# Optimization experiments

Measured on AMD Instinct MI355X. Metric: run time of the kernel, lower is better.

Reference implementation:

```python
import jax, jax.numpy as jnp
import numpy as np

PROX_THRESH = 50.0
NEG_SLOPE = 0.2  # PyG GATConv default leaky_relu slope


def _layer_norm(x, g, b, eps=1e-5):
    m = x.mean(-1, keepdims=True)
    v = x.var(-1, keepdims=True)
    return (x - m) / jnp.sqrt(v + eps) * g + b


def _forward(ego_agent_past, neighbor_agents_past, node_w, node_b, node_ln_g,
             node_ln_b, ego_w, ego_b, ego_ln_g, ego_ln_b, gat_w, gat_asrc,
             gat_adst, gat_b, proj_w, proj_b):
    B = ego_agent_past.shape[0]
    ego_last = ego_agent_past[:, -1, :5]            # [B,5]
    nbr_last = neighbor_agents_past[:, :, -1, :5]   # [B,Nn,5]
    x = jnp.concatenate([ego_last[:, None], nbr_last], axis=1)  # [B,N,5]
    N = x.shape[1]
    dim = node_w.shape[1]
    heads, C = gat_asrc.shape[1], gat_asrc.shape[2]

    # build_graph: edge (j->i) iff dist(i,j) < 50 and i != j; GATConv then
    # adds self-loops, so the diagonal is always connected.
    pos = x[..., :2]
    d2 = jnp.sum((pos[:, :, None, :] - pos[:, None, :, :]) ** 2, axis=-1)  # [B,N,N]
    eye = jnp.eye(N, dtype=bool)
    adj = ((jnp.sqrt(d2) < PROX_THRESH) & ~eye) | eye   # adj[b,i,j]: msg j -> i

    # node features zero-padded from 5 -> 11 columns (as in forward)
    nf = jnp.pad(x, ((0, 0), (0, 0), (0, 11 - x.shape[-1])))
    h_node = _layer_norm(jax.nn.relu(nf @ node_w + node_b), node_ln_g, node_ln_b)
    h_ego = _layer_norm(jax.nn.relu(nf[..., :7] @ ego_w + ego_b), ego_ln_g, ego_ln_b)
    is_ego = (jnp.arange(N) == 0)  # node 0 of every scene is the ego
    h = jnp.where(is_ego[None, :, None], h_ego, h_node)  # [B,N,dim]

    # GATConv layers (eval mode, dropout inactive), concat=True
    for l in range(gat_w.shape[0]):
        wh = (h @ gat_w[l]).reshape(B, N, heads, C)                    # [B,N,H,C]
        a_s = jnp.einsum('bnhc,hc->bnh', wh, gat_asrc[l])              # source term
        a_d = jnp.einsum('bnhc,hc->bnh', wh, gat_adst[l])              # dest term
        # e[b,i,j,h] for edge j->i
        e = jax.nn.leaky_relu(a_s[:, None, :, :] + a_d[:, :, None, :], NEG_SLOPE)
        e = jnp.where(adj[..., None], e, -1e9)
        alpha = jax.nn.softmax(e, axis=2)                              # over sources j
        out = jnp.einsum('bijh,bjhc->bihc', alpha, wh).reshape(B, N, dim) + gat_b[l]
        h = jax.nn.relu(out)

    h = h @ proj_w + proj_b
    # all agents are valid (randn features have nonzero abs-sum), so no padding
    mask = jnp.zeros((B, N), dtype=bool)
    return h, mask


def setup_inputs() -> dict:
    key = jax.random.key(0)
    ks = jax.random.split(key, 10)
    B, Nn, T = 16, 1023, 20
    dim, heads, L = 256, 4, 2
    C = dim // heads
    f = lambda i, s: jax.random.normal(ks[i], s, dtype=jnp.float32)
    return {
        'ego_agent_past': f(0, (B, T, 7)),
        'neighbor_agents_past': f(1, (B, Nn, T, 11)),
        'node_w': f(2, (11, dim)) * 0.1, 'node_b': jnp.zeros((dim,), jnp.float32),
        'node_ln_g': jnp.ones((dim,), jnp.float32), 'node_ln_b': jnp.zeros((dim,), jnp.float32),
        'ego_w': f(3, (7, dim)) * 0.1, 'ego_b': jnp.zeros((dim,), jnp.float32),
        'ego_ln_g': jnp.ones((dim,), jnp.float32), 'ego_ln_b': jnp.zeros((dim,), jnp.float32),
        'gat_w': f(4, (L, dim, dim)) * 0.1,
        'gat_asrc': f(5, (L, heads, C)) * 0.1,
        'gat_adst': f(6, (L, heads, C)) * 0.1,
        'gat_b': jnp.zeros((L, dim), jnp.float32),
        'proj_w': f(7, (dim, dim)) * 0.1, 'proj_b': jnp.zeros((dim,), jnp.float32),
    }


def reference(ego_agent_past, neighbor_agents_past, node_w, node_b, node_ln_g,
              node_ln_b, ego_w, ego_b, ego_ln_g, ego_ln_b, gat_w, gat_asrc,
              gat_adst, gat_b, proj_w, proj_b):
    return _forward(ego_agent_past, neighbor_agents_past, node_w, node_b,
                    node_ln_g, node_ln_b, ego_w, ego_b, ego_ln_g, ego_ln_b,
                    gat_w, gat_asrc, gat_adst, gat_b, proj_w, proj_b)
```

## Files before the change

kernel.cpp:

```cpp
#include <hip/hip_runtime.h>
#include <cstddef>

typedef _Float16 f16;
typedef _Float16 f16x8 __attribute__((ext_vector_type(8)));
typedef _Float16 f16x4 __attribute__((ext_vector_type(4)));
typedef __fp16 fp16x2 __attribute__((ext_vector_type(2)));
typedef float f32x4 __attribute__((ext_vector_type(4)));

#define BATCH 16
#define NAGENT 1024
#define NNBR 1023
#define TSTEP 20
#define DIM 256
#define ROWS 16384
#define TH2 2500.0f
#define LOG2E 1.44269504089f

#define O_PX   0
#define O_PY   16384
#define O_H16  32768
#define O_AS   2129920
#define O_AD   2195456
#define O_M    2260992
#define O_US   2261056
#define O_UD   2263104
#define O_WT   2265152
#define O_ADJ  2363456

__global__ __launch_bounds__(256) void node_embed(
    const float* __restrict__ ego, const float* __restrict__ nbr,
    const float* __restrict__ node_w, const float* __restrict__ node_b,
    const float* __restrict__ node_g, const float* __restrict__ node_beta,
    const float* __restrict__ ego_w, const float* __restrict__ ego_b,
    const float* __restrict__ ego_g, const float* __restrict__ ego_beta,
    f16* __restrict__ h16, float* __restrict__ px, float* __restrict__ py) {
    int w = threadIdx.x >> 6, lane = threadIdx.x & 63;
    int row = blockIdx.x * 4 + w;
    int b = row >> 10, n = row & 1023;
    const float* src;
    if (n == 0) src = ego + (size_t)b * TSTEP * 7 + (TSTEP - 1) * 7;
    else        src = nbr + (((size_t)b * NNBR + (n - 1)) * TSTEP + (TSTEP - 1)) * 11;
    const float *W, *bias, *g, *beta;
    if (n == 0) { W = ego_w;  bias = ego_b;  g = ego_g;  beta = ego_beta; }
    else        { W = node_w; bias = node_b; g = node_g; beta = node_beta; }
    float xv[5];
#pragma unroll
    for (int k = 0; k < 5; k++) xv[k] = src[k];
    if (lane == 0) { px[row] = xv[0]; py[row] = xv[1]; }
    int c0 = lane * 4;
    float4 bv = *(const float4*)(bias + c0);
    float acc[4] = {bv.x, bv.y, bv.z, bv.w};
#pragma unroll
    for (int k = 0; k < 5; k++) {
        float4 wv = *(const float4*)(W + (size_t)k * 256 + c0);
        acc[0] = fmaf(xv[k], wv.x, acc[0]);
        acc[1] = fmaf(xv[k], wv.y, acc[1]);
        acc[2] = fmaf(xv[k], wv.z, acc[2]);
        acc[3] = fmaf(xv[k], wv.w, acc[3]);
    }
#pragma unroll
    for (int c = 0; c < 4; c++) acc[c] = fmaxf(acc[c], 0.f);
    float s1 = acc[0] + acc[1] + acc[2] + acc[3];
    float s2 = acc[0]*acc[0] + acc[1]*acc[1] + acc[2]*acc[2] + acc[3]*acc[3];
#pragma unroll
    for (int off = 1; off < 64; off <<= 1) {
        s1 += __shfl_xor(s1, off);
        s2 += __shfl_xor(s2, off);
    }
    float mean = s1 * (1.f / 256.f);
    float var  = s2 * (1.f / 256.f) - mean * mean;
    float rstd = rsqrtf(var + 1e-5f);
    float4 gv = *(const float4*)(g + c0);
    float4 be = *(const float4*)(beta + c0);
    f16x4 o;
    o[0] = (f16)((acc[0] - mean) * rstd * gv.x + be.x);
    o[1] = (f16)((acc[1] - mean) * rstd * gv.y + be.y);
    o[2] = (f16)((acc[2] - mean) * rstd * gv.z + be.z);
    o[3] = (f16)((acc[3] - mean) * rstd * gv.w + be.w);
    *(f16x4*)(h16 + (size_t)row * 256 + c0) = o;
}

__global__ __launch_bounds__(256) void adj_build(const float* __restrict__ px,
                                                 const float* __restrict__ py,
                                                 unsigned char* __restrict__ mask) {
    int blk = blockIdx.x;
    int b = blk >> 6, ic = blk & 63;
    int base = b << 10;
    __shared__ float sx[1024], sy[1024];
    int t = threadIdx.x;
#pragma unroll
    for (int i = 0; i < 4; i++) {
        sx[t + i * 256] = px[base + t + i * 256];
        sy[t + i * 256] = py[base + t + i * 256];
    }
    __syncthreads();
    int i_loc = t >> 4;
    int s = (t >> 3) & 1;
    int q = (t >> 1) & 3;
    int chalf = t & 1;
    int ig = ic * 16 + i_loc;
    float xi = sx[ig], yi = sy[ig];
    unsigned int w0 = 0, w1 = 0;
#pragma unroll
    for (int cc = 0; cc < 8; cc++) {
        int c = chalf * 8 + cc;
        unsigned int byte = 0;
        int j0 = s * 512 + c * 32 + q * 8;
#pragma unroll
        for (int jj = 0; jj < 8; jj++) {
            int j = j0 + jj;
            float dx = sx[j] - xi, dy = sy[j] - yi;
            if ((dx * dx + dy * dy < TH2) || (j == ig)) byte |= 1u << jj;
        }
        if (cc < 4) w0 |= byte << (cc * 8);
        else        w1 |= byte << ((cc - 4) * 8);
    }
    uint2 v; v.x = w0; v.y = w1;
    *(uint2*)(mask + (((size_t)(base + ig)) << 7) + s * 64 + q * 16 + chalf * 8) = v;
}

__global__ __launch_bounds__(256) void prep_weights(
    const float* __restrict__ gat_w, const float* __restrict__ proj_w,
    const float* __restrict__ asrc, const float* __restrict__ adst,
    f16* __restrict__ WT, float* __restrict__ us, float* __restrict__ ud) {
    int bid = blockIdx.x;
    int t = threadIdx.x;
    if (bid < 48) {
        int m = bid >> 4, part = bid & 15;
        const float* W = (m < 2) ? (gat_w + (size_t)m * 65536) : proj_w;
        f16* WO = WT + (size_t)m * 65536;
#pragma unroll
        for (int i = 0; i < 2; i++) {
            int chunk = part * 512 + i * 256 + t;
            int lane = chunk & 63;
            int ksnt = chunk >> 6;
            int ks = ksnt & 7, nt = ksnt >> 3;
            int n = nt * 16 + (lane & 15);
            int k0 = ks * 32 + (lane >> 4) * 8;
            f16x8 v;
#pragma unroll
            for (int e = 0; e < 8; e++) v[e] = (f16)W[(size_t)(k0 + e) * 256 + n];
            *(f16x8*)(WO + (size_t)chunk * 8) = v;
        }
    } else {
        int blk = bid - 48;
        int l = blk >> 2, h = blk & 3;
        const float* W  = gat_w + (size_t)l * 65536 + t * 256 + h * 64;
        const float* as = asrc + l * 256 + h * 64;
        const float* ad = adst + l * 256 + h * 64;
        float s = 0.f, d = 0.f;
#pragma unroll 8
        for (int c = 0; c < 64; c++) { s = fmaf(W[c], as[c], s); d = fmaf(W[c], ad[c], d); }
        us[blk * 256 + t] = s;
        ud[blk * 256 + t] = d;
    }
}

__global__ __launch_bounds__(256, 4) void gemm_f16(
    const f16* __restrict__ A, const f16* __restrict__ BT2,
    f16* __restrict__ whT, float* __restrict__ outF, const float* __restrict__ bias,
    const float* __restrict__ us, const float* __restrict__ ud,
    float* __restrict__ a_sT, float* __restrict__ a_dT) {
    __shared__ f16 sA[32 * 264];
    __shared__ float sU[8 * 256];
    int t = threadIdx.x;
    int m0 = blockIdx.x * 32;
    {
        int r = t >> 3, u0 = (t & 7) * 4;
        const f16* gp = A + (size_t)(m0 + r) * 256 + u0 * 8;
        f16* lp = sA + r * 264 + u0 * 8;
#pragma unroll
        for (int u = 0; u < 4; u++)
            *(f16x8*)(lp + u * 8) = *(const f16x8*)(gp + u * 8);
    }
    if (us) {
#pragma unroll
        for (int i = 0; i < 4; i++) sU[t + i * 256] = us[t + i * 256];
#pragma unroll
        for (int i = 0; i < 4; i++) sU[1024 + t + i * 256] = ud[t + i * 256];
    }
    __syncthreads();
    int w = t >> 6, lane = t & 63, il = lane & 15, q = lane >> 4;
    int n0 = w * 64;
    f32x4 acc[2][4];
#pragma unroll
    for (int mt = 0; mt < 2; mt++)
#pragma unroll
        for (int nt = 0; nt < 4; nt++) acc[mt][nt] = (f32x4){0.f, 0.f, 0.f, 0.f};
    const f16* Bp  = BT2 + (size_t)w * 16384 + (size_t)lane * 8;
    const f16* Ap0 = sA + il * 264 + q * 8;
#pragma unroll 2
    for (int ksi = 0; ksi < 8; ksi++) {
        f16x8 a0 = *(const f16x8*)(Ap0 + ksi * 32);
        f16x8 a1 = *(const f16x8*)(Ap0 + 16 * 264 + ksi * 32);
        f16x8 b0 = *(const f16x8*)(Bp + ksi * 512);
        f16x8 b1 = *(const f16x8*)(Bp + 4096 + ksi * 512);
        f16x8 b2 = *(const f16x8*)(Bp + 8192 + ksi * 512);
        f16x8 b3 = *(const f16x8*)(Bp + 12288 + ksi * 512);
        acc[0][0] = __builtin_amdgcn_mfma_f32_16x16x32_f16(a0, b0, acc[0][0], 0, 0, 0);
        acc[0][1] = __builtin_amdgcn_mfma_f32_16x16x32_f16(a0, b1, acc[0][1], 0, 0, 0);
        acc[0][2] = __builtin_amdgcn_mfma_f32_16x16x32_f16(a0, b2, acc[0][2], 0, 0, 0);
        acc[0][3] = __builtin_amdgcn_mfma_f32_16x16x32_f16(a0, b3, acc[0][3], 0, 0, 0);
        acc[1][0] = __builtin_amdgcn_mfma_f32_16x16x32_f16(a1, b0, acc[1][0], 0, 0, 0);
        acc[1][1] = __builtin_amdgcn_mfma_f32_16x16x32_f16(a1, b1, acc[1][1], 0, 0, 0);
        acc[1][2] = __builtin_amdgcn_mfma_f32_16x16x32_f16(a1, b2, acc[1][2], 0, 0, 0);
        acc[1][3] = __builtin_amdgcn_mfma_f32_16x16x32_f16(a1, b3, acc[1][3], 0, 0, 0);
    }
    if (whT) {
        size_t tbase = ((size_t)blockIdx.x) * 512 + (size_t)(w * 4) * 512 * 512 + (size_t)(lane & 15) * 0;
#pragma unroll
        for (int mt = 0; mt < 2; mt++)
#pragma unroll
            for (int nt = 0; nt < 4; nt++) {
                f16x4 v;
#pragma unroll
                for (int reg = 0; reg < 4; reg++) v[reg] = (f16)acc[mt][nt][reg];
                size_t off = ((size_t)(w * 4 + nt) * 512 + blockIdx.x) * 512
                           + (size_t)((mt * 2 + (q >> 1)) * 16 + il) * 8 + (q & 1) * 4;
                *(f16x4*)(whT + off) = v;
            }
        (void)tbase;
    } else {
#pragma unroll
        for (int nt = 0; nt < 4; nt++) {
            float bv = bias[n0 + nt * 16 + il];
#pragma unroll
            for (int mt = 0; mt < 2; mt++)
#pragma unroll
                for (int reg = 0; reg < 4; reg++)
                    outF[(size_t)(m0 + mt * 16 + q * 4 + reg) * 256 + n0 + nt * 16 + il] =
                        acc[mt][nt][reg] + bv;
        }
    }
    if (us) {
        int r2 = t >> 3, sub = t & 7;
        int hh = sub & 3, isD = sub >> 2;
        const float* uv = sU + isD * 1024 + hh * 256;
        const f16* ar = sA + r2 * 264;
        float d0 = 0.f;
#pragma unroll 4
        for (int kk = 0; kk < 32; kk++) {
            f16x8 av = *(const f16x8*)(ar + kk * 8);
            float4 u0 = *(const float4*)(uv + kk * 8);
            float4 u1 = *(const float4*)(uv + kk * 8 + 4);
            d0 += (float)av[0] * u0.x + (float)av[1] * u0.y +
                  (float)av[2] * u0.z + (float)av[3] * u0.w +
                  (float)av[4] * u1.x + (float)av[5] * u1.y +
                  (float)av[6] * u1.z + (float)av[7] * u1.w;
        }
        float* dst = isD ? a_dT : a_sT;
        dst[(size_t)hh * ROWS + m0 + r2] = d0;
    }
}

__global__ __launch_bounds__(256) void reduce_max(const float* __restrict__ a_sT,
                                                  float* __restrict__ M) {
    int blk = blockIdx.x;
    int b = blk >> 2, h = blk & 3;
    const float* p = a_sT + (size_t)h * ROWS + b * NAGENT;
    int t = threadIdx.x;
    float m = fmaxf(fmaxf(p[t], p[t + 256]), fmaxf(p[t + 512], p[t + 768]));
#pragma unroll
    for (int off = 32; off > 0; off >>= 1) m = fmaxf(m, __shfl_down(m, off));
    __shared__ float red[4];
    if ((t & 63) == 0) red[t >> 6] = m;
    __syncthreads();
    if (t == 0) M[blk] = fmaxf(fmaxf(red[0], red[1]), fmaxf(red[2], red[3]));
}

__global__ __launch_bounds__(512, 4) void gat_attn(
    const f16* __restrict__ whT, const float* __restrict__ a_sT,
    const float* __restrict__ a_dT, const unsigned char* __restrict__ mask,
    const float* __restrict__ M, const float* __restrict__ gat_b,
    f16* __restrict__ h16out) {
    __shared__ f32x4 comb[10][4][64];
    int t = threadIdx.x;
    int w = t >> 6, lane = t & 63;
    int h = w & 3, s = w >> 2;
    int B = blockIdx.x;
    int slot = B >> 3;
    int b = (B & 7) + 8 * (slot >> 5);
    int i0 = (slot & 31) << 5;
    int base = b << 10;
    int il = lane & 15, q = lane >> 4;
    int ig0 = i0 + il, ig1 = i0 + 16 + il;

    float Mh = M[b * 4 + h];
    float adv0 = a_dT[(size_t)h * ROWS + base + ig0];
    float adv1 = a_dT[(size_t)h * ROWS + base + ig1];
    float mz0 = Mh + adv0, mz1 = Mh + adv1;
    float mi0 = fmaxf(mz0, 0.2f * mz0), mi1 = fmaxf(mz1, 0.2f * mz1);
    float nm0 = -mi0 * LOG2E, nm1 = -mi1 * LOG2E;

    uint4 mq0 = *(const uint4*)(mask + (((size_t)(base + ig0)) << 7) + s * 64 + q * 16);
    uint4 mq1 = *(const uint4*)(mask + (((size_t)(base + ig1)) << 7) + s * 64 + q * 16);
    unsigned int mw0[4] = {mq0.x, mq0.y, mq0.z, mq0.w};
    unsigned int mw1[4] = {mq1.x, mq1.y, mq1.z, mq1.w};

    f32x4 acc[2][5];
#pragma unroll
    for (int mt = 0; mt < 2; mt++)
#pragma unroll
        for (int nt = 0; nt < 5; nt++) acc[mt][nt] = (f32x4){0.f, 0.f, 0.f, 0.f};
    f16x8 ones;
#pragma unroll
    for (int j = 0; j < 8; j++) ones[j] = (f16)1.f;

    const f16*   wpb = whT + ((size_t)(h * 4) * 512 + b * 32 + s * 16) * 512 + (size_t)lane * 8;
    const float* asp = a_sT + (size_t)h * ROWS + base + (s << 9) + q * 8;

    for (int c = 0; c < 16; ++c) {
        f16x8 b0 = *(const f16x8*)(wpb + c * 512);
        f16x8 b1 = *(const f16x8*)(wpb + 262144 + c * 512);
        f16x8 b2 = *(const f16x8*)(wpb + 524288 + c * 512);
        f16x8 b3 = *(const f16x8*)(wpb + 786432 + c * 512);
        int j0 = c * 32;
        float4 as0 = *(const float4*)(asp + j0);
        float4 as1 = *(const float4*)(asp + j0 + 4);
        unsigned int mb0 = (mw0[c >> 2] >> ((c & 3) * 8)) & 255u;
        unsigned int mb1 = (mw1[c >> 2] >> ((c & 3) * 8)) & 255u;
        float asv[8] = {as0.x, as0.y, as0.z, as0.w, as1.x, as1.y, as1.z, as1.w};
        union { f16x8 v; fp16x2 hp[4]; } u0, u1;
#pragma unroll
        for (int jp = 0; jp < 4; ++jp) {
            float va = asv[2 * jp], vb = asv[2 * jp + 1];
            float za = va + adv0, zb = vb + adv0;
            float zc = va + adv1, zd = vb + adv1;
            float sa = fmaxf(za, 0.2f * za), sb = fmaxf(zb, 0.2f * zb);
            float sc_ = fmaxf(zc, 0.2f * zc), sd = fmaxf(zd, 0.2f * zd);
            float ea = exp2f(fmaf(sa, LOG2E, nm0));
            float eb = exp2f(fmaf(sb, LOG2E, nm0));
            float ec = exp2f(fmaf(sc_, LOG2E, nm1));
            float ed = exp2f(fmaf(sd, LOG2E, nm1));
            ea = ((mb0 >> (2 * jp)) & 1u) ? ea : 0.f;
            eb = ((mb0 >> (2 * jp + 1)) & 1u) ? eb : 0.f;
            ec = ((mb1 >> (2 * jp)) & 1u) ? ec : 0.f;
            ed = ((mb1 >> (2 * jp + 1)) & 1u) ? ed : 0.f;
            u0.hp[jp] = __builtin_amdgcn_cvt_pkrtz(ea, eb);
            u1.hp[jp] = __builtin_amdgcn_cvt_pkrtz(ec, ed);
        }
        f16x8 afr0 = u0.v, afr1 = u1.v;
        acc[0][0] = __builtin_amdgcn_mfma_f32_16x16x32_f16(afr0, b0, acc[0][0], 0, 0, 0);
        acc[1][0] = __builtin_amdgcn_mfma_f32_16x16x32_f16(afr1, b0, acc[1][0], 0, 0, 0);
        acc[0][1] = __builtin_amdgcn_mfma_f32_16x16x32_f16(afr0, b1, acc[0][1], 0, 0, 0);
        acc[1][1] = __builtin_amdgcn_mfma_f32_16x16x32_f16(afr1, b1, acc[1][1], 0, 0, 0);
        acc[0][2] = __builtin_amdgcn_mfma_f32_16x16x32_f16(afr0, b2, acc[0][2], 0, 0, 0);
        acc[1][2] = __builtin_amdgcn_mfma_f32_16x16x32_f16(afr1, b2, acc[1][2], 0, 0, 0);
        acc[0][3] = __builtin_amdgcn_mfma_f32_16x16x32_f16(afr0, b3, acc[0][3], 0, 0, 0);
        acc[1][3] = __builtin_amdgcn_mfma_f32_16x16x32_f16(afr1, b3, acc[1][3], 0, 0, 0);
        acc[0][4] = __builtin_amdgcn_mfma_f32_16x16x32_f16(afr0, ones, acc[0][4], 0, 0, 0);
        acc[1][4] = __builtin_amdgcn_mfma_f32_16x16x32_f16(afr1, ones, acc[1][4], 0, 0, 0);
    }
    if (s == 1) {
#pragma unroll
        for (int mt = 0; mt < 2; mt++)
#pragma unroll
            for (int nt = 0; nt < 5; nt++) comb[mt * 5 + nt][h][lane] = acc[mt][nt];
    }
    __syncthreads();
    if (s == 0) {
#pragma unroll
        for (int mt = 0; mt < 2; mt++)
#pragma unroll
            for (int nt = 0; nt < 5; nt++) acc[mt][nt] += comb[mt * 5 + nt][h][lane];
        float b0v = gat_b[h * 64 + il];
        float b1v = gat_b[h * 64 + 16 + il];
        float b2v = gat_b[h * 64 + 32 + il];
        float b3v = gat_b[h * 64 + 48 + il];
#pragma unroll
        for (int mt = 0; mt < 2; mt++) {
#pragma unroll
            for (int reg = 0; reg < 4; ++reg) {
                float inv = 1.f / acc[mt][4][reg];
                size_t ro = (size_t)(base + i0 + mt * 16 + q * 4 + reg) * DIM + h * 64 + il;
                h16out[ro +  0] = (f16)fmaxf(fmaf(acc[mt][0][reg], inv, b0v), 0.f);
                h16out[ro + 16] = (f16)fmaxf(fmaf(acc[mt][1][reg], inv, b1v), 0.f);
                h16out[ro + 32] = (f16)fmaxf(fmaf(acc[mt][2][reg], inv, b2v), 0.f);
                h16out[ro + 48] = (f16)fmaxf(fmaf(acc[mt][3][reg], inv, b3v), 0.f);
            }
        }
    }
}

__global__ void zero_mask(float* __restrict__ p) {
    p[blockIdx.x * 256 + threadIdx.x] = 0.f;
}

extern "C" void kernel_launch(void* const* d_in, const int* in_sizes, int n_in,
                              void* d_out, int out_size, void* d_ws, size_t ws_size,
                              hipStream_t stream) {
    const float* ego       = (const float*)d_in[0];
    const float* nbr       = (const float*)d_in[1];
    const float* node_w    = (const float*)d_in[2];
    const float* node_b    = (const float*)d_in[3];
    const float* node_g    = (const float*)d_in[4];
    const float* node_beta = (const float*)d_in[5];
    const float* ego_w     = (const float*)d_in[6];
    const float* ego_b     = (const float*)d_in[7];
    const float* ego_g     = (const float*)d_in[8];
    const float* ego_beta  = (const float*)d_in[9];
    const float* gat_w     = (const float*)d_in[10];
    const float* gat_asrc  = (const float*)d_in[11];
    const float* gat_adst  = (const float*)d_in[12];
    const float* gat_bias  = (const float*)d_in[13];
    const float* proj_w    = (const float*)d_in[14];
    const float* proj_b    = (const float*)d_in[15];

    float* out = (float*)d_out;
    float* ws  = (float*)d_ws;
    float* px   = ws + O_PX;
    float* py   = ws + O_PY;
    f16*   h16  = (f16*)(ws + O_H16);
    float* asT  = ws + O_AS;
    float* adT  = ws + O_AD;
    float* Mmax = ws + O_M;
    float* us   = ws + O_US;
    float* ud   = ws + O_UD;
    f16*   WT   = (f16*)(ws + O_WT);
    unsigned char* adj = (unsigned char*)(ws + O_ADJ);
    f16*   whT  = (f16*)d_out;

    node_embed<<<4096, 256, 0, stream>>>(ego, nbr, node_w, node_b, node_g, node_beta,
                                         ego_w, ego_b, ego_g, ego_beta, h16, px, py);
    adj_build<<<1024, 256, 0, stream>>>(px, py, adj);
    prep_weights<<<56, 256, 0, stream>>>(gat_w, proj_w, gat_asrc, gat_adst, WT, us, ud);
    for (int l = 0; l < 2; l++) {
        gemm_f16<<<512, 256, 0, stream>>>(h16, WT + (size_t)l * 65536, whT, nullptr, nullptr,
                                          us + l * 1024, ud + l * 1024, asT, adT);
        reduce_max<<<64, 256, 0, stream>>>(asT, Mmax);
        gat_attn<<<512, 512, 0, stream>>>(whT, asT, adT, adj, Mmax,
                                          gat_bias + l * 256, h16);
    }
    gemm_f16<<<512, 256, 0, stream>>>(h16, WT + (size_t)2 * 65536, nullptr, out, proj_b,
                                      nullptr, nullptr, nullptr, nullptr);
    zero_mask<<<64, 256, 0, stream>>>(out + (size_t)ROWS * DIM);
}
```

Measured before the change: 240.5 us.

## Factor GAT attention exponentials into precomputed per-source and per-destination terms

Because leaky_relu is piecewise linear, the exponent of each attention logit splits into a per-source exponential times a per-destination factor, with one pair for each branch. A new prep kernel precomputes exp(a_s - M) and exp(0.2*(a_s - M)) per source node alongside the max. The attention kernel then picks a branch with a comparison and does a multiply, so the inner loop no longer evaluates an exponential for every (i, j) pair. In exchange, each step reads two extra float arrays from memory, and products of small factors may lose some precision.

```diff
diff --git a/kernel.cpp b/kernel.cpp
--- a/kernel.cpp
+++ b/kernel.cpp
@@ -26,6 +26,8 @@
 #define O_UD   2263104
 #define O_WT   2265152
 #define O_ADJ  2363456
+#define O_EA   2887744
+#define O_EB   2953280
 
 __global__ __launch_bounds__(256) void node_embed(
     const float* __restrict__ ego, const float* __restrict__ nbr,
@@ -207,7 +209,6 @@
         acc[1][3] = __builtin_amdgcn_mfma_f32_16x16x32_f16(a1, b3, acc[1][3], 0, 0, 0);
     }
     if (whT) {
-        size_t tbase = ((size_t)blockIdx.x) * 512 + (size_t)(w * 4) * 512 * 512 + (size_t)(lane & 15) * 0;
 #pragma unroll
         for (int mt = 0; mt < 2; mt++)
 #pragma unroll
@@ -219,7 +220,6 @@
                            + (size_t)((mt * 2 + (q >> 1)) * 16 + il) * 8 + (q & 1) * 4;
                 *(f16x4*)(whT + off) = v;
             }
-        (void)tbase;
     } else {
 #pragma unroll
         for (int nt = 0; nt < 4; nt++) {
@@ -253,24 +253,46 @@
     }
 }
 
-__global__ __launch_bounds__(256) void reduce_max(const float* __restrict__ a_sT,
-                                                  float* __restrict__ M) {
+__global__ __launch_bounds__(256) void softmax_prep(const float* __restrict__ a_sT,
+                                                    float* __restrict__ M,
+                                                    float* __restrict__ EA,
+                                                    float* __restrict__ EB) {
     int blk = blockIdx.x;
     int b = blk >> 2, h = blk & 3;
-    const float* p = a_sT + (size_t)h * ROWS + b * NAGENT;
+    size_t off = (size_t)h * ROWS + b * NAGENT;
+    const float* p = a_sT + off;
     int t = threadIdx.x;
-    float m = fmaxf(fmaxf(p[t], p[t + 256]), fmaxf(p[t + 512], p[t + 768]));
-#pragma unroll
-    for (int off = 32; off > 0; off >>= 1) m = fmaxf(m, __shfl_down(m, off));
+    float v0 = p[t], v1 = p[t + 256], v2 = p[t + 512], v3 = p[t + 768];
+    float m = fmaxf(fmaxf(v0, v1), fmaxf(v2, v3));
+#pragma unroll
+    for (int o = 32; o > 0; o >>= 1) m = fmaxf(m, __shfl_down(m, o));
     __shared__ float red[4];
+    __shared__ float mfin;
     if ((t & 63) == 0) red[t >> 6] = m;
     __syncthreads();
-    if (t == 0) M[blk] = fmaxf(fmaxf(red[0], red[1]), fmaxf(red[2], red[3]));
+    if (t == 0) {
+        float mm = fmaxf(fmaxf(red[0], red[1]), fmaxf(red[2], red[3]));
+        M[blk] = mm;
+        mfin = mm;
+    }
+    __syncthreads();
+    float Mh = mfin;
+    float* ea = EA + off;
+    float* eb = EB + off;
+    ea[t]       = exp2f((v0 - Mh) * LOG2E);
+    ea[t + 256] = exp2f((v1 - Mh) * LOG2E);
+    ea[t + 512] = exp2f((v2 - Mh) * LOG2E);
+    ea[t + 768] = exp2f((v3 - Mh) * LOG2E);
+    eb[t]       = exp2f(0.2f * (v0 - Mh) * LOG2E);
+    eb[t + 256] = exp2f(0.2f * (v1 - Mh) * LOG2E);
+    eb[t + 512] = exp2f(0.2f * (v2 - Mh) * LOG2E);
+    eb[t + 768] = exp2f(0.2f * (v3 - Mh) * LOG2E);
 }
 
 __global__ __launch_bounds__(512, 4) void gat_attn(
     const f16* __restrict__ whT, const float* __restrict__ a_sT,
-    const float* __restrict__ a_dT, const unsigned char* __restrict__ mask,
+    const float* __restrict__ a_dT, const float* __restrict__ EA,
+    const float* __restrict__ EB, const unsigned char* __restrict__ mask,
     const float* __restrict__ M, const float* __restrict__ gat_b,
     f16* __restrict__ h16out) {
     __shared__ f32x4 comb[10][4][64];
@@ -290,7 +312,11 @@
     float adv1 = a_dT[(size_t)h * ROWS + base + ig1];
     float mz0 = Mh + adv0, mz1 = Mh + adv1;
     float mi0 = fmaxf(mz0, 0.2f * mz0), mi1 = fmaxf(mz1, 0.2f * mz1);
-    float nm0 = -mi0 * LOG2E, nm1 = -mi1 * LOG2E;
+    float fa0 = exp2f((mz0 - mi0) * LOG2E);
+    float fb0 = exp2f((0.2f * mz0 - mi0) * LOG2E);
+    float fa1 = exp2f((mz1 - mi1) * LOG2E);
+    float fb1 = exp2f((0.2f * mz1 - mi1) * LOG2E);
+    float nadv0 = -adv0, nadv1 = -adv1;
 
     uint4 mq0 = *(const uint4*)(mask + (((size_t)(base + ig0)) << 7) + s * 64 + q * 16);
     uint4 mq1 = *(const uint4*)(mask + (((size_t)(base + ig1)) << 7) + s * 64 + q * 16);
@@ -307,7 +333,10 @@
     for (int j = 0; j < 8; j++) ones[j] = (f16)1.f;
 
     const f16*   wpb = whT + ((size_t)(h * 4) * 512 + b * 32 + s * 16) * 512 + (size_t)lane * 8;
-    const float* asp = a_sT + (size_t)h * ROWS + base + (s << 9) + q * 8;
+    size_t joff = (size_t)h * ROWS + base + (s << 9) + q * 8;
+    const float* asp = a_sT + joff;
+    const float* eap = EA + joff;
+    const float* ebp = EB + joff;
 
     for (int c = 0; c < 16; ++c) {
         f16x8 b0 = *(const f16x8*)(wpb + c * 512);
@@ -317,27 +346,25 @@
         int j0 = c * 32;
         float4 as0 = *(const float4*)(asp + j0);
         float4 as1 = *(const float4*)(asp + j0 + 4);
+        float4 ea0 = *(const float4*)(eap + j0);
+        float4 ea1 = *(const float4*)(eap + j0 + 4);
+        float4 eb0 = *(const float4*)(ebp + j0);
+        float4 eb1 = *(const float4*)(ebp + j0 + 4);
         unsigned int mb0 = (mw0[c >> 2] >> ((c & 3) * 8)) & 255u;
         unsigned int mb1 = (mw1[c >> 2] >> ((c & 3) * 8)) & 255u;
         float asv[8] = {as0.x, as0.y, as0.z, as0.w, as1.x, as1.y, as1.z, as1.w};
+        float eav[8] = {ea0.x, ea0.y, ea0.z, ea0.w, ea1.x, ea1.y, ea1.z, ea1.w};
+        float ebv[8] = {eb0.x, eb0.y, eb0.z, eb0.w, eb1.x, eb1.y, eb1.z, eb1.w};
         union { f16x8 v; fp16x2 hp[4]; } u0, u1;
 #pragma unroll
         for (int jp = 0; jp < 4; ++jp) {
-            float va = asv[2 * jp], vb = asv[2 * jp + 1];
-            float za = va + adv0, zb = vb + adv0;
-            float zc = va + adv1, zd = vb + adv1;
-            float sa = fmaxf(za, 0.2f * za), sb = fmaxf(zb, 0.2f * zb);
-            float sc_ = fmaxf(zc, 0.2f * zc), sd = fmaxf(zd, 0.2f * zd);
-            float ea = exp2f(fmaf(sa, LOG2E, nm0));
-            float eb = exp2f(fmaf(sb, LOG2E, nm0));
-            float ec = exp2f(fmaf(sc_, LOG2E, nm1));
-            float ed = exp2f(fmaf(sd, LOG2E, nm1));
-            ea = ((mb0 >> (2 * jp)) & 1u) ? ea : 0.f;
-            eb = ((mb0 >> (2 * jp + 1)) & 1u) ? eb : 0.f;
-            ec = ((mb1 >> (2 * jp)) & 1u) ? ec : 0.f;
-            ed = ((mb1 >> (2 * jp + 1)) & 1u) ? ed : 0.f;
-            u0.hp[jp] = __builtin_amdgcn_cvt_pkrtz(ea, eb);
-            u1.hp[jp] = __builtin_amdgcn_cvt_pkrtz(ec, ed);
+            int ja = 2 * jp, jb = 2 * jp + 1;
+            float pa0 = ((mb0 >> ja) & 1u) ? ((asv[ja] > nadv0) ? eav[ja] * fa0 : ebv[ja] * fb0) : 0.f;
+            float pb0 = ((mb0 >> jb) & 1u) ? ((asv[jb] > nadv0) ? eav[jb] * fa0 : ebv[jb] * fb0) : 0.f;
+            float pa1 = ((mb1 >> ja) & 1u) ? ((asv[ja] > nadv1) ? eav[ja] * fa1 : ebv[ja] * fb1) : 0.f;
+            float pb1 = ((mb1 >> jb) & 1u) ? ((asv[jb] > nadv1) ? eav[jb] * fa1 : ebv[jb] * fb1) : 0.f;
+            u0.hp[jp] = __builtin_amdgcn_cvt_pkrtz(pa0, pb0);
+            u1.hp[jp] = __builtin_amdgcn_cvt_pkrtz(pa1, pb1);
         }
         f16x8 afr0 = u0.v, afr1 = u1.v;
         acc[0][0] = __builtin_amdgcn_mfma_f32_16x16x32_f16(afr0, b0, acc[0][0], 0, 0, 0);
@@ -418,6 +445,8 @@
     float* ud   = ws + O_UD;
     f16*   WT   = (f16*)(ws + O_WT);
     unsigned char* adj = (unsigned char*)(ws + O_ADJ);
+    float* EAb  = ws + O_EA;
+    float* EBb  = ws + O_EB;
     f16*   whT  = (f16*)d_out;
 
     node_embed<<<4096, 256, 0, stream>>>(ego, nbr, node_w, node_b, node_g, node_beta,
@@ -427,8 +456,8 @@
     for (int l = 0; l < 2; l++) {
         gemm_f16<<<512, 256, 0, stream>>>(h16, WT + (size_t)l * 65536, whT, nullptr, nullptr,
                                           us + l * 1024, ud + l * 1024, asT, adT);
-        reduce_max<<<64, 256, 0, stream>>>(asT, Mmax);
-        gat_attn<<<512, 512, 0, stream>>>(whT, asT, adT, adj, Mmax,
+        softmax_prep<<<64, 256, 0, stream>>>(asT, Mmax, EAb, EBb);
+        gat_attn<<<512, 512, 0, stream>>>(whT, asT, adT, EAb, EBb, adj, Mmax,
                                           gat_bias + l * 256, h16);
     }
     gemm_f16<<<512, 256, 0, stream>>>(h16, WT + (size_t)2 * 65536, nullptr, out, proj_b,
```

Result: faster. 228.1 us (-5.2%).
